# Kernel tuning notes

Hardware: AMD Instinct MI355X
Metric: run time of the kernel (lower is better)

## Reference

```python
import jax, jax.numpy as jnp
import numpy as np

B, NX, NT, W, M = 4, 512, 128, 64, 16
EPS = 1e-5


def setup_inputs() -> dict:
    key = jax.random.key(0)
    ks = jax.random.split(key, 13)
    scale = 1.0 / (W * W)  # torch: scale * torch.rand(..., cfloat) -> U[0,1) real & imag
    return {
        "x": jax.random.normal(ks[0], (B, NX, NT, W), jnp.float32),
        "grid": jnp.linspace(0.0, 1.0, NX, dtype=jnp.float32),
        "pole_re": scale * jax.random.uniform(ks[1], (W, W, M), jnp.float32),
        "pole_im": scale * jax.random.uniform(ks[2], (W, W, M), jnp.float32),
        "res_re": scale * jax.random.uniform(ks[3], (W, W, M), jnp.float32),
        "res_im": scale * jax.random.uniform(ks[4], (W, W, M), jnp.float32),
        "conv_w": jax.random.normal(ks[5], (W, W), jnp.float32) / np.sqrt(W),
        "conv_b": jax.random.normal(ks[6], (W,), jnp.float32) * 0.02,
        "gru_Wx": jax.random.normal(ks[7], (3 * W, W), jnp.float32) / np.sqrt(W),
        "gru_Wh": jax.random.normal(ks[8], (3 * W, W), jnp.float32) / np.sqrt(W),
        "gru_bx": jax.random.normal(ks[9], (3 * W,), jnp.float32) * 0.02,
        "gru_bh": jax.random.normal(ks[10], (3 * W,), jnp.float32) * 0.02,
        "out_W": jax.random.normal(ks[11], (W, W), jnp.float32) / np.sqrt(W),
        "out_b": jax.random.normal(ks[12], (W,), jnp.float32) * 0.02,
    }


def instance_norm(v):
    # torch InstanceNorm1d (affine=False, biased var) over last dim; v: [N, C, L]
    mu = v.mean(-1, keepdims=True)
    var = ((v - mu) ** 2).mean(-1, keepdims=True)
    return (v - mu) * jax.lax.rsqrt(var + EPS)


def pr_forward(xs, grid, pole, residue):
    # xs: [BT, W, Nx]; pole/residue: [in, out, modes] complex64
    nx = xs.shape[-1]
    dt = grid[1] - grid[0]
    alpha = jnp.fft.fft(xs)  # [BT, W, Nx] complex64
    lam = 1j * (2.0 * np.pi) * jnp.fft.fftfreq(nx, dt).astype(jnp.float32)  # [Nx]
    Hw = residue / (lam[:, None, None, None] - pole)  # [Nx, i, o, m]
    or1 = jnp.einsum('bix,xiom->box', alpha, Hw)       # [BT, W, Nx]
    or2 = -jnp.einsum('bix,xiom->bom', alpha, Hw)      # [BT, W, M]
    x1 = jnp.real(jnp.fft.ifft(or1, n=nx))
    # exp of outer product pole (x) grid: [i, o, m, Nx]
    term2 = jnp.exp(pole[..., None] * grid.astype(jnp.complex64)[None, None, None, :])
    # faithful to torch einsum 'bix,ioxz->boz': or2 channel contracts with term2's in-dim
    x2 = jnp.real(jnp.einsum('bim,iomz->boz', or2, term2)) / nx
    return x1 + x2


def gru(xseq, Wx, Wh, bx, bh):
    # xseq: [N, T, D] -> [N, T, H]; torch nn.GRU gate order (r, z, n)
    H = Wh.shape[1]
    gx = xseq @ Wx.T + bx  # precompute input gates [N, T, 3H]

    def step(h, g):
        gh = h @ Wh.T + bh
        xr, xz, xn = jnp.split(g, 3, axis=-1)
        hr, hz, hn = jnp.split(gh, 3, axis=-1)
        r = jax.nn.sigmoid(xr + hr)
        z = jax.nn.sigmoid(xz + hz)
        n = jnp.tanh(xn + r * hn)
        h = (1.0 - z) * n + z * h
        return h, h

    h0 = jnp.zeros((xseq.shape[0], H), xseq.dtype)
    _, hs = jax.lax.scan(step, h0, gx.transpose(1, 0, 2))
    return hs.transpose(1, 0, 2)


def reference(x, grid, pole_re, pole_im, res_re, res_im, conv_w, conv_b,
              gru_Wx, gru_Wh, gru_bx, gru_bh, out_W, out_b):
    b, nx, nt, w = x.shape
    xs = x.transpose(0, 2, 3, 1).reshape(b * nt, w, nx)  # [B*Nt, W, Nx]
    pole = pole_re + 1j * pole_im
    residue = res_re + 1j * res_im
    x1 = instance_norm(pr_forward(instance_norm(xs), grid, pole, residue))
    x2 = jnp.einsum('oi,bin->bon', conv_w, xs) + conv_b[None, :, None]  # Conv1d k=1
    h = jnp.sin(x1 + x2)
    h = h.reshape(b, nt, w, nx).transpose(0, 3, 1, 2).reshape(b * nx, nt, w)
    y = gru(h, gru_Wx, gru_Wh, gru_bx, gru_bh) @ out_W.T + out_b
    return y.reshape(b, nx, nt, w)
```

## Files before the change

### kernel.cpp

```cpp
#include <hip/hip_runtime.h>
#include <math.h>

#define PI2F 6.283185307179586f
typedef unsigned short ushort_t;

__device__ inline ushort_t f2bf(float f) {
  unsigned u = __float_as_uint(f);
  unsigned r = (u + 0x7FFFu + ((u >> 16) & 1u)) >> 16;
  return (ushort_t)r;
}
__device__ inline float bf2f(ushort_t u) {
  return __uint_as_float(((unsigned)u) << 16);
}


__global__ __launch_bounds__(256) void k1a_transpose(const float* __restrict__ x,
                                                     float* __restrict__ xs) {
  const int bt = blockIdx.x >> 2, nt4 = blockIdx.x & 3;
  const int b = bt >> 7, t = bt & 127;
  const int n0 = nt4 * 128;
  __shared__ float tile[128 * 66];
  const int tid = threadIdx.x;
  const int i = tid & 63, nq = tid >> 6;
  const float* xb = x + (size_t)b * 4194304 + (size_t)t * 64;
  for (int k = 0; k < 32; k++) {
    int nl = nq + 4 * k;
    tile[nl * 66 + i] = xb[(size_t)(n0 + nl) * 8192 + i];
  }
  __syncthreads();
  float* dst = xs + (size_t)bt * 32768;
  for (int idx = tid; idx < 8192; idx += 256) {
    int ii = idx >> 7, nl = idx & 127;
    dst[ii * 512 + n0 + nl] = tile[nl * 66 + ii];
  }
}

__global__ __launch_bounds__(64) void k2_fft(const float* __restrict__ xs,
                                             float2* __restrict__ alpha,
                                             float2* __restrict__ a0,
                                             float2* __restrict__ a256,
                                             float2* __restrict__ s1o,
                                             float2* __restrict__ s2o,
                                             const float* __restrict__ grd) {
  __shared__ float2 bufA[512], bufB[512], tw[256];
  const int s = blockIdx.x, tid = threadIdx.x;
  const float dt = grd[1] - grd[0];
  const float Ndt = 512.f * dt;
  for (int m = tid; m < 256; m += 64) {
    float ang = -PI2F * (float)m * (1.f / 512.f);
    float sv, cv; sincosf(ang, &sv, &cv);
    tw[m].x = cv; tw[m].y = sv;
  }
  const float* src = xs + (size_t)s * 512;
  float v[8]; float sm = 0.f, sq = 0.f;
#pragma unroll
  for (int k = 0; k < 8; k++) { v[k] = src[tid + 64 * k]; sm += v[k]; sq += v[k] * v[k]; }
#pragma unroll
  for (int off = 32; off; off >>= 1) { sm += __shfl_down(sm, off); sq += __shfl_down(sq, off); }
  sm = __shfl(sm, 0); sq = __shfl(sq, 0);
  float mu = sm * (1.f / 512.f);
  float var = sq * (1.f / 512.f) - mu * mu;
  float rs = rsqrtf(var + 1e-5f);
#pragma unroll
  for (int k = 0; k < 8; k++) { bufA[tid + 64 * k].x = (v[k] - mu) * rs; bufA[tid + 64 * k].y = 0.f; }
  __syncthreads();
  float2* sp = bufA; float2* dp = bufB;
  int Ns = 1;
  for (int st = 0; st < 9; st++) {
    const int shift = 8 - st;
    for (int jj = 0; jj < 4; jj++) {
      int j = tid + 64 * jj;
      int r = j & (Ns - 1);
      float2 a = sp[j], b = sp[j + 256];
      float2 w = tw[r << shift];
      float wbx = w.x * b.x - w.y * b.y;
      float wby = w.x * b.y + w.y * b.x;
      int id = ((j >> st) << (st + 1)) + r;
      dp[id].x = a.x + wbx; dp[id].y = a.y + wby;
      dp[id + Ns].x = a.x - wbx; dp[id + Ns].y = a.y - wby;
    }
    __syncthreads();
    float2* tp = sp; sp = dp; dp = tp;
    Ns <<= 1;
  }
  float2* dst = alpha + (size_t)s * 256;
  float s1x = 0.f, s1y = 0.f, s2x = 0.f, s2y = 0.f;
  for (int k = tid; k < 512; k += 64) {
    float2 vv = sp[k];
    if (k < 256) dst[k] = vv;
    if (k != 0) {
      int kk = (k < 256) ? k : k - 512;
      float invL = Ndt / (PI2F * (float)kk);
      s1x += vv.y * invL; s1y -= vv.x * invL;
      float invL2 = invL * invL;
      s2x -= vv.x * invL2; s2y -= vv.y * invL2;
    }
  }
#pragma unroll
  for (int off = 32; off; off >>= 1) {
    s1x += __shfl_down(s1x, off); s1y += __shfl_down(s1y, off);
    s2x += __shfl_down(s2x, off); s2y += __shfl_down(s2y, off);
  }
  if (tid == 0) {
    s1o[s].x = s1x; s1o[s].y = s1y;
    s2o[s].x = s2x; s2o[s].y = s2y;
    a0[s] = sp[0];
    a256[s] = sp[256];
  }
}

__global__ __launch_bounds__(64) void k3a_R(const float* __restrict__ pre, const float* __restrict__ pim,
                                            const float* __restrict__ rre, const float* __restrict__ rim,
                                            float2* __restrict__ R0, float2* __restrict__ R1,
                                            float2* __restrict__ R2,
                                            float* __restrict__ Pm, float* __restrict__ Qm,
                                            float* __restrict__ ptr_re, float* __restrict__ ptr_im) {
  const int i = blockIdx.x, o = threadIdx.x;
  float r0x = 0, r0y = 0, r1x = 0, r1y = 0, r2x = 0, r2y = 0;
  for (int m = 0; m < 16; m++) {
    size_t idx = ((size_t)i * 64 + o) * 16 + m;
    float px = pre[idx], py = pim[idx];
    float rx = rre[idx], ry = rim[idx];
    r1x += rx; r1y += ry;
    r2x += rx * px - ry * py; r2y += rx * py + ry * px;
    float inv = 1.f / (px * px + py * py);
    r0x -= (rx * px + ry * py) * inv;
    r0y -= (ry * px - rx * py) * inv;
    ptr_re[((size_t)i * 16 + m) * 64 + o] = px;
    ptr_im[((size_t)i * 16 + m) * 64 + o] = py;
  }
  R0[i * 64 + o].x = r0x; R0[i * 64 + o].y = r0y;
  R1[i * 64 + o].x = r1x; R1[i * 64 + o].y = r1y;
  R2[i * 64 + o].x = r2x; R2[i * 64 + o].y = r2y;
  Pm[i * 64 + o] = 2.f * r1x;
  Qm[i * 64 + o] = 2.f * r2x;
}

__global__ __launch_bounds__(1024) void k3b_or2(const float* __restrict__ pre, const float* __restrict__ pim,
                                                const float* __restrict__ rre, const float* __restrict__ rim,
                                                const float2* __restrict__ a0, const float2* __restrict__ s1,
                                                const float2* __restrict__ s2, float2* __restrict__ or2) {
  const int bt = blockIdx.x;
  __shared__ float2 A0[64], S1[64], S2[64];
  const int tid = threadIdx.x;
  if (tid < 64) { A0[tid] = a0[bt * 64 + tid]; S1[tid] = s1[bt * 64 + tid]; S2[tid] = s2[bt * 64 + tid]; }
  __syncthreads();
  float ax = 0.f, ay = 0.f;
  for (int i = 0; i < 64; i++) {
    size_t idx = (size_t)i * 1024 + tid;
    float px = pre[idx], py = pim[idx];
    float rx = rre[idx], ry = rim[idx];
    float inv = 1.f / (px * px + py * py);
    float q0x = -(rx * px + ry * py) * inv;
    float q0y = -(ry * px - rx * py) * inv;
    float2 a0v = A0[i], s1v = S1[i], s2v = S2[i];
    float tx = q0x * a0v.x - q0y * a0v.y + rx * s1v.x - ry * s1v.y;
    float ty = q0x * a0v.y + q0y * a0v.x + rx * s1v.y + ry * s1v.x;
    float rpx = rx * px - ry * py, rpy = rx * py + ry * px;
    tx += rpx * s2v.x - rpy * s2v.y;
    ty += rpx * s2v.y + rpy * s2v.x;
    ax -= tx; ay -= ty;
  }
  or2[(size_t)bt * 1024 + tid].x = ax;
  or2[(size_t)bt * 1024 + tid].y = ay;
}

__global__ __launch_bounds__(256) void k3c_T(const float2* __restrict__ or2,
                                             const float* __restrict__ ptr_re, const float* __restrict__ ptr_im,
                                             const float2* __restrict__ R0, const float2* __restrict__ R1,
                                             const float2* __restrict__ R2,
                                             const float2* __restrict__ a0, const float2* __restrict__ a256,
                                             float* __restrict__ T0, float* __restrict__ T1,
                                             float* __restrict__ T2,
                                             float* __restrict__ or10re, float* __restrict__ r256o,
                                             const float* __restrict__ grd) {
  const int bt = blockIdx.x * 4 + (threadIdx.x >> 6);
  const int o = threadIdx.x & 63;
  const float dt = grd[1] - grd[0];
  const float invL256 = -(512.f * dt) / (PI2F * 256.f);
  float ox = 0.f;
  float c1x = 0.f, c1y = 0.f, c2x = 0.f, c2y = 0.f;
  for (int i = 0; i < 64; i++) {
    float2 av = a0[bt * 64 + i];
    float2 rv = R0[i * 64 + o];
    ox += av.x * rv.x - av.y * rv.y;
    float2 aw = a256[bt * 64 + i];
    float2 r1v = R1[i * 64 + o], r2v = R2[i * 64 + o];
    c1x += aw.x * r1v.x - aw.y * r1v.y;
    c1y += aw.x * r1v.y + aw.y * r1v.x;
    c2x += aw.x * r2v.x - aw.y * r2v.y;
    c2y += aw.x * r2v.y + aw.y * r2v.x;
  }
  or10re[bt * 64 + o] = ox;
  r256o[bt * 64 + o] = invL256 * (c1y - invL256 * c2x);
  float t0 = 0.f, t1 = 0.f, t2 = 0.f;
  for (int im = 0; im < 1024; im++) {
    float2 c = or2[(size_t)bt * 1024 + im];
    float px = ptr_re[(size_t)im * 64 + o], py = ptr_im[(size_t)im * 64 + o];
    t0 += c.x;
    t1 += c.x * px - c.y * py;
    float p2x = px * px - py * py, p2y = 2.f * px * py;
    t2 += c.x * p2x - c.y * p2y;
  }
  T1[bt * 64 + o] = t1; T2[bt * 64 + o] = t2;
  if (o == 0) T0[bt] = t0;
}

__global__ __launch_bounds__(256) void k4_or1(float2* __restrict__ alpha,
                                              const float* __restrict__ Pm, const float* __restrict__ Qm,
                                              const float* __restrict__ or10re, const float* __restrict__ r256o,
                                              const float* __restrict__ grd) {
  const int bt = blockIdx.x >> 2, xc = blockIdx.x & 3;
  const int x0 = xc * 64;
  __shared__ float aRe[64][68], aIm[64][68];
  const int tid = threadIdx.x;
  const float dt = grd[1] - grd[0];
  const float Ndt = 512.f * dt;
  float2* base = alpha + (size_t)bt * 16384;
  for (int idx = tid; idx < 4096; idx += 256) {
    int ii = idx >> 6, xl = idx & 63;
    float2 v = base[ii * 256 + x0 + xl];
    aRe[ii][xl] = v.x; aIm[ii][xl] = v.y;
  }
  __syncthreads();
  const int xq = tid & 15, oq = tid >> 4;
  const int xb = xq * 4, ob = oq * 4;
  float c1r[4][4] = {}, c1i[4][4] = {}, c2r[4][4] = {}, c2i[4][4] = {};
#pragma unroll 4
  for (int i = 0; i < 64; i++) {
    float4 ar = *(const float4*)&aRe[i][xb];
    float4 ai = *(const float4*)&aIm[i][xb];
    float4 pv = *(const float4*)&Pm[i * 64 + ob];
    float4 qv = *(const float4*)&Qm[i * 64 + ob];
    float pa[4] = {pv.x, pv.y, pv.z, pv.w};
    float qa[4] = {qv.x, qv.y, qv.z, qv.w};
    float arr[4] = {ar.x, ar.y, ar.z, ar.w};
    float aii[4] = {ai.x, ai.y, ai.z, ai.w};
#pragma unroll
    for (int a = 0; a < 4; a++) {
#pragma unroll
      for (int c = 0; c < 4; c++) {
        c1r[a][c] += arr[c] * pa[a];
        c1i[a][c] += aii[c] * pa[a];
        c2r[a][c] += arr[c] * qa[a];
        c2i[a][c] += aii[c] * qa[a];
      }
    }
  }
#pragma unroll
  for (int a = 0; a < 4; a++) {
    int o = ob + a;
    float2* orow = base + o * 256 + x0;
#pragma unroll
    for (int c = 0; c < 4; c++) {
      int gx = x0 + xb + c;
      float re, im;
      if (gx == 0) {
        re = or10re[bt * 64 + o];
        im = r256o[bt * 64 + o];
      } else {
        float invL = Ndt / (PI2F * (float)gx);
        re = invL * (c1i[a][c] - invL * c2r[a][c]);
        im = -invL * (c1r[a][c] + invL * c2i[a][c]);
      }
      orow[xb + c].x = re; orow[xb + c].y = im;
    }
  }
}

__global__ __launch_bounds__(64) void k5_ifft(const float2* __restrict__ G,
                                              float* __restrict__ x1,
                                              const float* __restrict__ T0, const float* __restrict__ T1,
                                              const float* __restrict__ T2, const float* __restrict__ grd) {
  __shared__ float2 bufA[512], bufB[512], tw[256];
  const int s = blockIdx.x, tid = threadIdx.x;
  const int bt = s >> 6;
  for (int m = tid; m < 256; m += 64) {
    float ang = PI2F * (float)m * (1.f / 512.f);
    float sv, cv; sincosf(ang, &sv, &cv);
    tw[m].x = cv; tw[m].y = sv;
  }
  const float2* src = G + (size_t)s * 256;
  float2 g0 = src[0];
  for (int k = tid; k < 512; k += 64) {
    float2 vv; vv.x = 0.f; vv.y = 0.f;
    if (k >= 1 && k < 256) vv = src[k];
    bufA[k] = vv;
  }
  __syncthreads();
  float2* sp = bufA; float2* dp = bufB;
  int Ns = 1;
  for (int st = 0; st < 9; st++) {
    const int shift = 8 - st;
    for (int jj = 0; jj < 4; jj++) {
      int j = tid + 64 * jj;
      int r = j & (Ns - 1);
      float2 a = sp[j], b = sp[j + 256];
      float2 w = tw[r << shift];
      float wbx = w.x * b.x - w.y * b.y;
      float wby = w.x * b.y + w.y * b.x;
      int id = ((j >> st) << (st + 1)) + r;
      dp[id].x = a.x + wbx; dp[id].y = a.y + wby;
      dp[id + Ns].x = a.x - wbx; dp[id + Ns].y = a.y - wby;
    }
    __syncthreads();
    float2* tp = sp; sp = dp; dp = tp;
    Ns <<= 1;
  }
  const float t0 = T0[bt], t1 = T1[s], t2 = T2[s];
  float* dst = x1 + (size_t)s * 512;
  for (int k = tid; k < 512; k += 64) {
    float g = grd[k];
    float sgn = (k & 1) ? -1.f : 1.f;
    dst[k] = (sp[k].x + g0.x + sgn * g0.y + t0 + t1 * g + 0.5f * t2 * g * g) * (1.f / 512.f);
  }
}

__global__ __launch_bounds__(256) void k6a_stats(const float* __restrict__ x1,
                                                 float* __restrict__ mu2, float* __restrict__ rs2) {
  const int row = blockIdx.x * 4 + (threadIdx.x >> 6);
  const int lane = threadIdx.x & 63;
  const float* p = x1 + (size_t)row * 512;
  float s = 0.f, s2 = 0.f;
#pragma unroll
  for (int k = 0; k < 8; k++) { float v = p[lane + 64 * k]; s += v; s2 += v * v; }
#pragma unroll
  for (int off = 32; off; off >>= 1) { s += __shfl_down(s, off); s2 += __shfl_down(s2, off); }
  if (lane == 0) {
    float mu = s * (1.f / 512.f);
    float var = s2 * (1.f / 512.f) - mu * mu;
    mu2[row] = mu;
    rs2[row] = rsqrtf(var + 1e-5f);
  }
}

__global__ __launch_bounds__(256) void k6b_assemble(const float* __restrict__ xsraw,
                                                    const float* __restrict__ x1,
                                                    const float* __restrict__ conv_w,
                                                    const float* __restrict__ conv_b,
                                                    const float* __restrict__ mu2, const float* __restrict__ rs2,
                                                    ushort_t* __restrict__ hseqb) {
  const int bt = blockIdx.x >> 2, nt4 = blockIdx.x & 3;
  const int b = bt >> 7, t = bt & 127;
  const int n0 = nt4 * 128;
  __shared__ float xt[128 * 66];
  __shared__ float wt[64 * 66];
  __shared__ float mun[64], rsn[64];
  const int tid = threadIdx.x;
  for (int idx = tid; idx < 4096; idx += 256) {
    int o = idx >> 6, ii = idx & 63;
    wt[o * 66 + ii] = conv_w[idx];
  }
  if (tid < 64) { mun[tid] = mu2[bt * 64 + tid]; rsn[tid] = rs2[bt * 64 + tid]; }
  const float* src = xsraw + (size_t)bt * 32768;
  for (int idx = tid; idx < 8192; idx += 256) {
    int ii = idx >> 7, nl = idx & 127;
    xt[nl * 66 + ii] = src[ii * 512 + n0 + nl];
  }
  __syncthreads();
  const int lane = tid & 63, og = tid >> 6;
  float acc[2][16];
  for (int half = 0; half < 2; half++) {
    int nl = lane + 64 * half;
#pragma unroll
    for (int j = 0; j < 16; j++) acc[half][j] = conv_b[og * 16 + j];
    const float2* xrow = (const float2*)&xt[nl * 66];
#pragma unroll 4
    for (int i2 = 0; i2 < 32; i2++) {
      float2 v = xrow[i2];
#pragma unroll
      for (int j = 0; j < 16; j++) {
        float2 wv = *(const float2*)&wt[(og * 16 + j) * 66 + 2 * i2];
        acc[half][j] += wv.x * v.x + wv.y * v.y;
      }
    }
  }
  const float* xb = x1 + (size_t)bt * 32768 + n0;
  for (int half = 0; half < 2; half++) {
    int nl = lane + 64 * half;
#pragma unroll
    for (int j = 0; j < 16; j++) {
      int o = og * 16 + j;
      float v = (xb[o * 512 + nl] - mun[o]) * rsn[o] + acc[half][j];
      acc[half][j] = sinf(v);
    }
  }
  __syncthreads();
  float* tile = xt;
  for (int half = 0; half < 2; half++) {
    int nl = lane + 64 * half;
#pragma unroll
    for (int j = 0; j < 16; j++) tile[(og * 16 + j) * 129 + nl] = acc[half][j];
  }
  __syncthreads();
  for (int idx = tid; idx < 8192; idx += 256) {
    int nl = idx >> 6, o = idx & 63;
    hseqb[(((size_t)(b * 512 + n0 + nl)) * 128 + t) * 64 + o] = f2bf(tile[o * 129 + nl]);
  }
}

__global__ __launch_bounds__(256) void k6c_xgemm(const ushort_t* __restrict__ hseqb,
                                                 const float* __restrict__ Wx, const float* __restrict__ bxv,
                                                 ushort_t* __restrict__ gxr, ushort_t* __restrict__ gxz,
                                                 ushort_t* __restrict__ gxn) {
  __shared__ float ht[64][68];
  __shared__ float wt[192][66];
  const int tid = threadIdx.x;
  const size_t rt0 = (size_t)blockIdx.x * 64;
  for (int idx = tid; idx < 12288; idx += 256) {
    int g = idx >> 6, c = idx & 63;
    wt[g][c] = Wx[idx];
  }
  for (int idx = tid; idx < 4096; idx += 256) {
    int rt = idx >> 6, c = idx & 63;
    ht[rt][c] = bf2f(hseqb[(rt0 + rt) * 64 + c]);
  }
  __syncthreads();
  const int a = tid & 15, bq = tid >> 4;
  float acc[4][12];
#pragma unroll
  for (int g = 0; g < 12; g++) {
    float bv = bxv[bq * 12 + g];
    acc[0][g] = bv; acc[1][g] = bv; acc[2][g] = bv; acc[3][g] = bv;
  }
  for (int c4 = 0; c4 < 16; c4++) {
    float4 h0 = *(const float4*)&ht[a][c4 * 4];
    float4 h1 = *(const float4*)&ht[a + 16][c4 * 4];
    float4 h2 = *(const float4*)&ht[a + 32][c4 * 4];
    float4 h3 = *(const float4*)&ht[a + 48][c4 * 4];
#pragma unroll
    for (int g = 0; g < 12; g++) {
      float4 wv = *(const float4*)&wt[bq * 12 + g][c4 * 4];
      acc[0][g] += h0.x * wv.x + h0.y * wv.y + h0.z * wv.z + h0.w * wv.w;
      acc[1][g] += h1.x * wv.x + h1.y * wv.y + h1.z * wv.z + h1.w * wv.w;
      acc[2][g] += h2.x * wv.x + h2.y * wv.y + h2.z * wv.z + h2.w * wv.w;
      acc[3][g] += h3.x * wv.x + h3.y * wv.y + h3.z * wv.z + h3.w * wv.w;
    }
  }
#pragma unroll
  for (int r = 0; r < 4; r++) {
    size_t rt = rt0 + a + 16 * r;
#pragma unroll
    for (int g = 0; g < 12; g++) {
      int gg = bq * 12 + g;
      ushort_t v = f2bf(acc[r][g]);
      ushort_t* dst = (gg < 64) ? gxr : ((gg < 128) ? gxz : gxn);
      dst[rt * 64 + (gg & 63)] = v;
    }
  }
}

__global__ __launch_bounds__(64, 2) void k7_gru(const ushort_t* __restrict__ gxr,
                                                const ushort_t* __restrict__ gxz,
                                                const ushort_t* __restrict__ gxn,
                                                const float* __restrict__ Wh,
                                                const float* __restrict__ bh,
                                                float* __restrict__ hist) {
  __shared__ float hx[64];
  const int row = blockIdx.x;
  const int j = threadIdx.x;
  float whr[64], whz[64], whn[64];
  {
    const float4* qr = (const float4*)(Wh + (size_t)j * 64);
    const float4* qz = (const float4*)(Wh + (size_t)(j + 64) * 64);
    const float4* qn = (const float4*)(Wh + (size_t)(j + 128) * 64);
#pragma unroll
    for (int c4 = 0; c4 < 16; c4++) {
      float4 v;
      v = qr[c4]; whr[4*c4]=v.x; whr[4*c4+1]=v.y; whr[4*c4+2]=v.z; whr[4*c4+3]=v.w;
      v = qz[c4]; whz[4*c4]=v.x; whz[4*c4+1]=v.y; whz[4*c4+2]=v.z; whz[4*c4+3]=v.w;
      v = qn[c4]; whn[4*c4]=v.x; whn[4*c4+1]=v.y; whn[4*c4+2]=v.z; whn[4*c4+3]=v.w;
    }
  }
  const float bhr = bh[j], bhz = bh[j + 64], bhn = bh[j + 128];
  const ushort_t* gr = gxr + (size_t)row * 8192;
  const ushort_t* gz = gxz + (size_t)row * 8192;
  const ushort_t* gn = gxn + (size_t)row * 8192;
  float* hrow = hist + (size_t)row * 8192;
  float h = 0.f;
  for (int t = 0; t < 128; t++) {
    float xr = bf2f(gr[t * 64 + j]);
    float xz = bf2f(gz[t * 64 + j]);
    float xn = bf2f(gn[t * 64 + j]);
    __syncthreads();
    hx[j] = h;
    __syncthreads();
    float aR = bhr, aZ = bhz, aN = bhn;
#pragma unroll
    for (int c4 = 0; c4 < 16; c4++) {
      float4 hv = *(const float4*)&hx[c4 * 4];
      aR += whr[4*c4] * hv.x + whr[4*c4+1] * hv.y + whr[4*c4+2] * hv.z + whr[4*c4+3] * hv.w;
      aZ += whz[4*c4] * hv.x + whz[4*c4+1] * hv.y + whz[4*c4+2] * hv.z + whz[4*c4+3] * hv.w;
      aN += whn[4*c4] * hv.x + whn[4*c4+1] * hv.y + whn[4*c4+2] * hv.z + whn[4*c4+3] * hv.w;
    }
    float r = 1.f / (1.f + __expf(-(xr + aR)));
    float z = 1.f / (1.f + __expf(-(xz + aZ)));
    float nv = xn + r * aN;
    float e2 = __expf(2.f * nv);
    float th = 1.f - 2.f / (e2 + 1.f);
    h = (1.f - z) * th + z * h;
    hrow[t * 64 + j] = h;
  }
}

__global__ __launch_bounds__(256) void k8_out(const float* __restrict__ hist,
                                              const float* __restrict__ outW, const float* __restrict__ outb,
                                              float* __restrict__ y) {
  __shared__ float ht[64 * 68];
  __shared__ float wl[4096];
  const int tid = threadIdx.x;
  const int rt0 = blockIdx.x * 64;
  for (int idx = tid; idx < 4096; idx += 256) wl[idx] = outW[idx];
  for (int idx = tid; idx < 4096; idx += 256) {
    int rt = idx >> 6, c = idx & 63;
    ht[rt * 68 + c] = hist[(size_t)(rt0 + rt) * 64 + c];
  }
  __syncthreads();
  const int j = tid & 63, rg = tid >> 6;
  float wj[64];
#pragma unroll
  for (int c = 0; c < 64; c++) wj[c] = wl[j * 64 + c];
  const float bj = outb[j];
  for (int k = 0; k < 16; k++) {
    int rt = rg + 4 * k;
    float acc = bj;
    const float4* hp = (const float4*)&ht[rt * 68];
#pragma unroll
    for (int c4 = 0; c4 < 16; c4++) {
      float4 hv = hp[c4];
      acc += wj[4 * c4] * hv.x + wj[4 * c4 + 1] * hv.y + wj[4 * c4 + 2] * hv.z + wj[4 * c4 + 3] * hv.w;
    }
    y[(size_t)(rt0 + rt) * 64 + j] = acc;
  }
}

extern "C" void kernel_launch(void* const* d_in, const int* in_sizes, int n_in,
                              void* d_out, int out_size, void* d_ws, size_t ws_size,
                              hipStream_t stream) {
  (void)in_sizes; (void)n_in; (void)out_size;
  const float* x      = (const float*)d_in[0];
  const float* grd    = (const float*)d_in[1];
  const float* pre    = (const float*)d_in[2];
  const float* pim    = (const float*)d_in[3];
  const float* rre    = (const float*)d_in[4];
  const float* rim    = (const float*)d_in[5];
  const float* conv_w = (const float*)d_in[6];
  const float* conv_b = (const float*)d_in[7];
  const float* gWx    = (const float*)d_in[8];
  const float* gWh    = (const float*)d_in[9];
  const float* gbx    = (const float*)d_in[10];
  const float* gbh    = (const float*)d_in[11];
  const float* outW   = (const float*)d_in[12];
  const float* outb   = (const float*)d_in[13];
  float* out = (float*)d_out;
  float* ws  = (float*)d_ws;

  if (ws_size < 52003328ULL * 4ULL) return;

  float*  XS = ws;
  float2* AH = (float2*)(ws + 16777216);
  float*  X1 = ws + 33554432;
  float*  sm = ws + 50331648;
  float2* A0    = (float2*)(sm + 0);
  float2* A256  = (float2*)(sm + 65536);
  float2* S1    = (float2*)(sm + 131072);
  float2* S2    = (float2*)(sm + 196608);
  float2* R0    = (float2*)(sm + 262144);
  float2* R1C   = (float2*)(sm + 270336);
  float2* R2C   = (float2*)(sm + 278528);
  float*  Pm    = sm + 286720;
  float*  Qm    = sm + 290816;
  float*  PTR   = sm + 294912;
  float*  PTI   = sm + 360448;
  float2* OR2   = (float2*)(sm + 425984);
  float*  T0    = sm + 1474560;
  float*  T1    = sm + 1475072;
  float*  T2    = sm + 1507840;
  float*  OR10R = sm + 1540608;
  float*  R256  = sm + 1573376;
  float*  MU2   = sm + 1606144;
  float*  RS2   = sm + 1638912;

  ushort_t* hseqb = (ushort_t*)AH;
  ushort_t* GXN   = (ushort_t*)AH + 16777216;
  ushort_t* GXR   = (ushort_t*)XS;
  ushort_t* GXZ   = (ushort_t*)XS + 16777216;
  float* hist = X1;

  k1a_transpose<<<2048, 256, 0, stream>>>(x, XS);
  k2_fft<<<32768, 64, 0, stream>>>(XS, AH, A0, A256, S1, S2, grd);
  k3a_R<<<64, 64, 0, stream>>>(pre, pim, rre, rim, R0, R1C, R2C, Pm, Qm, PTR, PTI);
  k3b_or2<<<512, 1024, 0, stream>>>(pre, pim, rre, rim, A0, S1, S2, OR2);
  k3c_T<<<128, 256, 0, stream>>>(OR2, PTR, PTI, R0, R1C, R2C, A0, A256, T0, T1, T2, OR10R, R256, grd);
  k4_or1<<<2048, 256, 0, stream>>>(AH, Pm, Qm, OR10R, R256, grd);
  k5_ifft<<<32768, 64, 0, stream>>>(AH, X1, T0, T1, T2, grd);
  k6a_stats<<<8192, 256, 0, stream>>>(X1, MU2, RS2);
  k6b_assemble<<<2048, 256, 0, stream>>>(XS, X1, conv_w, conv_b, MU2, RS2, hseqb);
  k6c_xgemm<<<4096, 256, 0, stream>>>(hseqb, gWx, gbx, GXR, GXZ, GXN);
  k7_gru<<<2048, 64, 0, stream>>>(GXR, GXZ, GXN, gWh, gbh, hist);
  k8_out<<<4096, 256, 0, stream>>>(hist, outW, outb, out);
}
```

Baseline: 1.178 ms.

## Split GRU recurrent matvec across three waves, one per gate

The GRU kernel now runs 192 threads per sequence instead of 64, so each thread holds one row of Wh (64 registers) rather than three gate rows (192 registers). Each wave computes one gate's recurrent dot product with four independent accumulators and writes it to shared memory. The first wave then applies the gate nonlinearities and updates h. The aim is to cut per-thread register pressure and shorten the serial per-step FMA chain by spreading it over more waves, at the cost of extra shared-memory traffic and an idle two-thirds of the block during the elementwise update.

```diff
diff --git a/kernel.cpp b/kernel.cpp
--- a/kernel.cpp
+++ b/kernel.cpp
@@ -450,56 +450,60 @@
   }
 }
 
-__global__ __launch_bounds__(64, 2) void k7_gru(const ushort_t* __restrict__ gxr,
-                                                const ushort_t* __restrict__ gxz,
-                                                const ushort_t* __restrict__ gxn,
-                                                const float* __restrict__ Wh,
-                                                const float* __restrict__ bh,
-                                                float* __restrict__ hist) {
+__global__ __launch_bounds__(192) void k7_gru(const ushort_t* __restrict__ gxr,
+                                              const ushort_t* __restrict__ gxz,
+                                              const ushort_t* __restrict__ gxn,
+                                              const float* __restrict__ Wh,
+                                              const float* __restrict__ bh,
+                                              float* __restrict__ hist) {
   __shared__ float hx[64];
+  __shared__ float ag[192], axv[192];
   const int row = blockIdx.x;
-  const int j = threadIdx.x;
-  float whr[64], whz[64], whn[64];
+  const int tid = threadIdx.x;
+  const int g = tid >> 6, j = tid & 63;
+  float w[64];
   {
-    const float4* qr = (const float4*)(Wh + (size_t)j * 64);
-    const float4* qz = (const float4*)(Wh + (size_t)(j + 64) * 64);
-    const float4* qn = (const float4*)(Wh + (size_t)(j + 128) * 64);
+    const float4* wp = (const float4*)(Wh + (size_t)tid * 64);
 #pragma unroll
     for (int c4 = 0; c4 < 16; c4++) {
-      float4 v;
-      v = qr[c4]; whr[4*c4]=v.x; whr[4*c4+1]=v.y; whr[4*c4+2]=v.z; whr[4*c4+3]=v.w;
-      v = qz[c4]; whz[4*c4]=v.x; whz[4*c4+1]=v.y; whz[4*c4+2]=v.z; whz[4*c4+3]=v.w;
-      v = qn[c4]; whn[4*c4]=v.x; whn[4*c4+1]=v.y; whn[4*c4+2]=v.z; whn[4*c4+3]=v.w;
-    }
-  }
-  const float bhr = bh[j], bhz = bh[j + 64], bhn = bh[j + 128];
-  const ushort_t* gr = gxr + (size_t)row * 8192;
-  const ushort_t* gz = gxz + (size_t)row * 8192;
-  const ushort_t* gn = gxn + (size_t)row * 8192;
+      float4 v = wp[c4];
+      w[4*c4] = v.x; w[4*c4+1] = v.y; w[4*c4+2] = v.z; w[4*c4+3] = v.w;
+    }
+  }
+  const float bias = bh[tid];
+  const ushort_t* gp = ((g == 0) ? gxr : (g == 1) ? gxz : gxn) + (size_t)row * 8192;
   float* hrow = hist + (size_t)row * 8192;
+  if (tid < 64) hx[tid] = 0.f;
+  __syncthreads();
   float h = 0.f;
   for (int t = 0; t < 128; t++) {
-    float xr = bf2f(gr[t * 64 + j]);
-    float xz = bf2f(gz[t * 64 + j]);
-    float xn = bf2f(gn[t * 64 + j]);
+    float xv = bf2f(gp[t * 64 + j]);
+    float a0 = 0.f, a1 = 0.f, a2 = 0.f, a3 = 0.f;
+#pragma unroll
+    for (int c4 = 0; c4 < 4; c4++) {
+      float4 h0 = *(const float4*)&hx[c4 * 16];
+      float4 h1 = *(const float4*)&hx[c4 * 16 + 4];
+      float4 h2 = *(const float4*)&hx[c4 * 16 + 8];
+      float4 h3 = *(const float4*)&hx[c4 * 16 + 12];
+      a0 += w[16*c4]    * h0.x + w[16*c4+1]  * h0.y + w[16*c4+2]  * h0.z + w[16*c4+3]  * h0.w;
+      a1 += w[16*c4+4]  * h1.x + w[16*c4+5]  * h1.y + w[16*c4+6]  * h1.z + w[16*c4+7]  * h1.w;
+      a2 += w[16*c4+8]  * h2.x + w[16*c4+9]  * h2.y + w[16*c4+10] * h2.z + w[16*c4+11] * h2.w;
+      a3 += w[16*c4+12] * h3.x + w[16*c4+13] * h3.y + w[16*c4+14] * h3.z + w[16*c4+15] * h3.w;
+    }
+    ag[tid] = bias + ((a0 + a1) + (a2 + a3));
+    axv[tid] = xv;
     __syncthreads();
-    hx[j] = h;
+    if (tid < 64) {
+      float r = 1.f / (1.f + __expf(-(ag[j] + axv[j])));
+      float z = 1.f / (1.f + __expf(-(ag[64 + j] + axv[64 + j])));
+      float nv = axv[128 + j] + r * ag[128 + j];
+      float e2 = __expf(2.f * nv);
+      float th = 1.f - 2.f / (e2 + 1.f);
+      h = (1.f - z) * th + z * h;
+      hx[j] = h;
+      hrow[t * 64 + j] = h;
+    }
     __syncthreads();
-    float aR = bhr, aZ = bhz, aN = bhn;
-#pragma unroll
-    for (int c4 = 0; c4 < 16; c4++) {
-      float4 hv = *(const float4*)&hx[c4 * 4];
-      aR += whr[4*c4] * hv.x + whr[4*c4+1] * hv.y + whr[4*c4+2] * hv.z + whr[4*c4+3] * hv.w;
-      aZ += whz[4*c4] * hv.x + whz[4*c4+1] * hv.y + whz[4*c4+2] * hv.z + whz[4*c4+3] * hv.w;
-      aN += whn[4*c4] * hv.x + whn[4*c4+1] * hv.y + whn[4*c4+2] * hv.z + whn[4*c4+3] * hv.w;
-    }
-    float r = 1.f / (1.f + __expf(-(xr + aR)));
-    float z = 1.f / (1.f + __expf(-(xz + aZ)));
-    float nv = xn + r * aN;
-    float e2 = __expf(2.f * nv);
-    float th = 1.f - 2.f / (e2 + 1.f);
-    h = (1.f - z) * th + z * h;
-    hrow[t * 64 + j] = h;
   }
 }
 
@@ -597,6 +601,6 @@
   k6a_stats<<<8192, 256, 0, stream>>>(X1, MU2, RS2);
   k6b_assemble<<<2048, 256, 0, stream>>>(XS, X1, conv_w, conv_b, MU2, RS2, hseqb);
   k6c_xgemm<<<4096, 256, 0, stream>>>(hseqb, gWx, gbx, GXR, GXZ, GXN);
-  k7_gru<<<2048, 64, 0, stream>>>(GXR, GXZ, GXN, gWh, gbh, hist);
+  k7_gru<<<2048, 192, 0, stream>>>(GXR, GXZ, GXN, gWh, gbh, hist);
   k8_out<<<4096, 256, 0, stream>>>(hist, outW, outb, out);
 }
```

After: 1.220 ms. 1.04x slower.
